# Performance work log

Measured on AMD Instinct MI355X. Metric: run time of the kernel, lower is better.

Reference implementation:

```python
import jax, jax.numpy as jnp
import numpy as np

N, E = 20000, 100000
D_IN, H1, C1 = 512, 8, 64   # conv1: 512 -> 8 heads x 64, concat -> 512
H2, C2 = 4, 128             # conv2: 512 -> 4 heads x 128, mean -> 128


def setup_inputs() -> dict:
    key = jax.random.key(0)
    k = jax.random.split(key, 12)
    s_in = 1.0 / np.sqrt(D_IN).astype(np.float32)
    return {
        "street_embedding": jax.random.normal(k[0], (N, D_IN), jnp.float32),
        "edge_index": jax.random.randint(k[1], (2, E), 0, N),
        "y": jax.random.randint(k[2], (N,), 0, C2),
        "train_mask": jax.random.bernoulli(k[3], 0.5, (N,)),
        "W1": jax.random.normal(k[4], (D_IN, H1 * C1), jnp.float32) * s_in,
        "att_src1": jax.random.normal(k[5], (H1, C1), jnp.float32) * 0.1,
        "att_dst1": jax.random.normal(k[6], (H1, C1), jnp.float32) * 0.1,
        "b1": jnp.zeros((H1 * C1,), jnp.float32),
        "W2": jax.random.normal(k[7], (H1 * C1, H2 * C2), jnp.float32) * s_in,
        "att_src2": jax.random.normal(k[8], (H2, C2), jnp.float32) * 0.1,
        "att_dst2": jax.random.normal(k[9], (H2, C2), jnp.float32) * 0.1,
        "b2": jnp.zeros((C2,), jnp.float32),
    }


def _gat_conv(x, W, a_src, a_dst, b, src, dst, n, H, C, concat):
    # linear transform (no bias, as in PyG GATConv's internal lin)
    xp = (x @ W).reshape(n, H, C)                      # [N,H,C]
    asrc = jnp.einsum('nhc,hc->nh', xp, a_src)         # [N,H]
    adst = jnp.einsum('nhc,hc->nh', xp, a_dst)
    e = jax.nn.leaky_relu(asrc[src] + adst[dst], 0.2)  # [E',H] edge scores
    # softmax over incoming edges per destination node
    m = jax.lax.stop_gradient(jax.ops.segment_max(e, dst, num_segments=n))
    ex = jnp.exp(e - m[dst])
    denom = jax.ops.segment_sum(ex, dst, num_segments=n)
    alpha = ex / (denom[dst] + 1e-16)                  # [E',H]
    out = jax.ops.segment_sum(alpha[:, :, None] * xp[src], dst, num_segments=n)  # [N,H,C]
    if concat:
        return out.reshape(n, H * C) + b
    return out.mean(axis=1) + b


def reference(street_embedding, edge_index, y, train_mask,
              W1, att_src1, att_dst1, b1, W2, att_src2, att_dst2, b2):
    n = street_embedding.shape[0]
    loop = jnp.arange(n)
    # PyG GATConv adds self-loops by default
    src = jnp.concatenate([edge_index[0], loop])
    dst = jnp.concatenate([edge_index[1], loop])
    # dropout layers are identity in eval mode
    h = _gat_conv(street_embedding, W1, att_src1, att_dst1, b1, src, dst, n, H1, C1, True)
    h = jax.nn.elu(h)
    out = _gat_conv(h, W2, att_src2, att_dst2, b2, src, dst, n, H2, C2, False)  # [N,C2]
    # CrossEntropyLoss, mean over train_mask nodes (weighted mean, jit-safe)
    logp = jax.nn.log_softmax(out, axis=-1)
    ce = -jnp.take_along_axis(logp, y[:, None], axis=-1)[:, 0]
    w = train_mask.astype(out.dtype)
    loss_su = jnp.sum(w * ce) / jnp.sum(w)
    return (loss_su, out)
```

## Files before the change

### kernel.cpp

```cpp
#include <hip/hip_runtime.h>
#include <cmath>

#define D_IN 512
#define HC   512
#define NH1  8
#define NC1  64
#define NH2  4
#define NC2  128
#define BM 128
#define BN 128
#define BK 64

typedef __attribute__((ext_vector_type(8))) short short8;
typedef __attribute__((ext_vector_type(4))) float f32x4;

__device__ inline ushort f2bf(float f) {
  unsigned u = __float_as_uint(f);
  return (ushort)((u + 0x7FFFu + ((u >> 16) & 1u)) >> 16);
}
__device__ inline float bf2f(ushort b) { return __uint_as_float(((unsigned)b) << 16); }

__global__ void k_cast_all(const float* __restrict__ x, ushort* __restrict__ Abf,
                           const float* __restrict__ W1, const float* __restrict__ W2,
                           ushort* __restrict__ Wt1, ushort* __restrict__ Wt2, int n4x) {
  const int KN = D_IN * HC;
  int i = blockIdx.x * blockDim.x + threadIdx.x;
  if (i < n4x) {
    float4 v = ((const float4*)x)[i];
    ushort4 r = { f2bf(v.x), f2bf(v.y), f2bf(v.z), f2bf(v.w) };
    ((ushort4*)Abf)[i] = r;
  } else {
    int idx = i - n4x;
    if (idx >= 2 * KN) return;
    const float* W = (idx < KN) ? W1 : W2;
    ushort* Wt = (idx < KN) ? Wt1 : Wt2;
    int j = (idx < KN) ? idx : idx - KN;
    int n = j / D_IN, k = j - n * D_IN;
    Wt[j] = f2bf(W[(size_t)k * HC + n]);
  }
}

template<int H>
__global__ void k_gemm_bf16(const ushort* __restrict__ A, const ushort* __restrict__ Bt,
                            ushort* __restrict__ Cbf,
                            const float* __restrict__ att_s, const float* __restrict__ att_d,
                            float* __restrict__ asrc, float* __restrict__ adst, int M) {
  constexpr int C = HC / H;
  __shared__ __align__(16) ushort As[BM * BK];
  __shared__ __align__(16) ushort Bs[BN * BK];
  int t = threadIdx.x;
  int m0 = blockIdx.y * BM;
  int n0 = blockIdx.x * BN;
  int wave = t >> 6, lane = t & 63;
  int ln = lane & 15, qd = lane >> 4;
  int wm = (wave >> 1) * 64, wn = (wave & 1) * 64;

  f32x4 acc[4][4] = {};

  int g = t >> 6, ct = (t >> 4) & 3, lt = t & 15;
  int rA0 = m0 + g * 16 + lt;      if (rA0 > M - 1) rA0 = M - 1;
  int rA1 = m0 + 64 + g * 16 + lt; if (rA1 > M - 1) rA1 = M - 1;
  const ushort* gA0 = A + (size_t)rA0 * D_IN + ct * 8;
  const ushort* gA1 = A + (size_t)rA1 * D_IN + ct * 8;
  const ushort* gB0 = Bt + (size_t)(n0 + g * 16 + lt) * D_IN + ct * 8;
  const ushort* gB1 = Bt + (size_t)(n0 + 64 + g * 16 + lt) * D_IN + ct * 8;

  for (int k0 = 0; k0 < D_IN; k0 += BK) {
    __syncthreads();
#pragma unroll
    for (int h = 0; h < 2; ++h) {
      int ko = k0 + h * 32;
      int lo = h * 4096;
      __builtin_amdgcn_global_load_lds(
          (const __attribute__((address_space(1))) void*)(gA0 + ko),
          (__attribute__((address_space(3))) void*)(As + lo + t * 8), 16, 0, 0);
      __builtin_amdgcn_global_load_lds(
          (const __attribute__((address_space(1))) void*)(gA1 + ko),
          (__attribute__((address_space(3))) void*)(As + lo + 2048 + t * 8), 16, 0, 0);
      __builtin_amdgcn_global_load_lds(
          (const __attribute__((address_space(1))) void*)(gB0 + ko),
          (__attribute__((address_space(3))) void*)(Bs + lo + t * 8), 16, 0, 0);
      __builtin_amdgcn_global_load_lds(
          (const __attribute__((address_space(1))) void*)(gB1 + ko),
          (__attribute__((address_space(3))) void*)(Bs + lo + 2048 + t * 8), 16, 0, 0);
    }
    __syncthreads();
#pragma unroll
    for (int h = 0; h < 2; ++h) {
      int lo = h * 4096;
      short8 a[4], bb[4];
#pragma unroll
      for (int i = 0; i < 4; ++i)
        a[i] = *(const short8*)&As[lo + (((wave >> 1) * 4 + i) * 4 + qd) * 128 + ln * 8];
#pragma unroll
      for (int j = 0; j < 4; ++j)
        bb[j] = *(const short8*)&Bs[lo + (((wave & 1) * 4 + j) * 4 + qd) * 128 + ln * 8];
#pragma unroll
      for (int i = 0; i < 4; ++i)
#pragma unroll
        for (int j = 0; j < 4; ++j)
          acc[i][j] = __builtin_amdgcn_mfma_f32_16x16x32_bf16(a[i], bb[j], acc[i][j], 0, 0, 0);
    }
  }

#pragma unroll
  for (int i = 0; i < 4; ++i) {
#pragma unroll
    for (int reg = 0; reg < 4; ++reg) {
      int row = m0 + wm + i * 16 + qd * 4 + reg;
      if (row >= M) continue;
#pragma unroll
      for (int j = 0; j < 4; ++j)
        Cbf[(size_t)row * HC + n0 + wn + j * 16 + ln] = f2bf(acc[i][j][reg]);
    }
  }

  int colbase = n0 + wn;
  int h = colbase / C;
  float sa[4], da[4];
#pragma unroll
  for (int j = 0; j < 4; ++j) {
    int c = (colbase % C) + j * 16 + ln;
    sa[j] = att_s[h * C + c];
    da[j] = att_d[h * C + c];
  }
#pragma unroll
  for (int i = 0; i < 4; ++i) {
#pragma unroll
    for (int reg = 0; reg < 4; ++reg) {
      float ps = acc[i][0][reg] * sa[0] + acc[i][1][reg] * sa[1]
               + acc[i][2][reg] * sa[2] + acc[i][3][reg] * sa[3];
      float pd = acc[i][0][reg] * da[0] + acc[i][1][reg] * da[1]
               + acc[i][2][reg] * da[2] + acc[i][3][reg] * da[3];
#pragma unroll
      for (int o = 1; o < 16; o <<= 1) { ps += __shfl_xor(ps, o); pd += __shfl_xor(pd, o); }
      int row = m0 + wm + i * 16 + qd * 4 + reg;
      if (ln == 0 && row < M) {
        if (C == 64) {
          asrc[row * H + h] = ps; adst[row * H + h] = pd;
        } else {
          int sub = (colbase >> 6) & 1;
          asrc[(row * H + h) * 2 + sub] = ps;
          adst[(row * H + h) * 2 + sub] = pd;
        }
      }
    }
  }
}

__global__ void k_hist(const int* __restrict__ ei, int E, int Etot, int* __restrict__ cnt) {
  int e = blockIdx.x * blockDim.x + threadIdx.x;
  if (e >= Etot) return;
  int d = (e < E) ? ei[E + e] : e - E;
  atomicAdd(&cnt[d], 1);
}

__global__ void k_scan(const int* __restrict__ cnt, int* __restrict__ rowstart, int N) {
  int tid = threadIdx.x;
  int T = (N + 1023) / 1024;
  int base = tid * T;
  int sum = 0;
  for (int i = 0; i < T; ++i) { int j = base + i; if (j < N) sum += cnt[j]; }
  int lane = tid & 63, w = tid >> 6;
  int v = sum;
#pragma unroll
  for (int off = 1; off < 64; off <<= 1) {
    int u = __shfl_up(v, off);
    if (lane >= off) v += u;
  }
  __shared__ int wsum[16];
  if (lane == 63) wsum[w] = v;
  __syncthreads();
  if (tid < 16) {
    int tv = wsum[tid];
#pragma unroll
    for (int off = 1; off < 16; off <<= 1) {
      int u = __shfl_up(tv, off);
      if (tid >= off) tv += u;
    }
    wsum[tid] = tv;
  }
  __syncthreads();
  int wave_prefix = (w == 0) ? 0 : wsum[w - 1];
  int run = wave_prefix + v - sum;
  for (int i = 0; i < T; ++i) {
    int j = base + i;
    if (j < N) { rowstart[j] = run; run += cnt[j]; }
  }
  if (tid == 1023) rowstart[N] = run;
}

__global__ void k_scatter(const int* __restrict__ ei, int E, int Etot,
                          const int* __restrict__ rowstart, int* __restrict__ cursor,
                          int* __restrict__ csr_src) {
  int e = blockIdx.x * blockDim.x + threadIdx.x;
  if (e >= Etot) return;
  int s = (e < E) ? ei[e] : e - E;
  int d = (e < E) ? ei[E + e] : e - E;
  int pos = atomicAdd(&cursor[d], 1);
  csr_src[rowstart[d] + pos] = s;
}

template<int H, int MODE>
__global__ void k_agg(const int* __restrict__ rowstart, const int* __restrict__ csr_src,
                      const float* __restrict__ asrc, const float* __restrict__ adst,
                      const ushort* __restrict__ xp, ushort* __restrict__ hout,
                      float* __restrict__ out2, const float* __restrict__ bias,
                      const int* __restrict__ y, const int* __restrict__ msk,
                      float* __restrict__ acc2, int N) {
  int n = blockIdx.x;
  int tid = threadIdx.x;
  constexpr int C = HC / H;
  int h = (tid * 4) / C;
  int beg = rowstart[n], end = rowstart[n + 1];

  __shared__ int   s_src[32];
  __shared__ float s_out[512];

  float adn = (MODE == 1) ? adst[n * H + h]
                          : adst[(n * H + h) * 2] + adst[(n * H + h) * 2 + 1];
  float ax = 0.f, ay = 0.f, az = 0.f, aw = 0.f, wsum = 0.f;

#define SCORE(s) ((MODE == 1) ? asrc[(s) * H + h] \
                              : asrc[((s) * H + h) * 2] + asrc[((s) * H + h) * 2 + 1])

  for (int c0 = beg; c0 < end; c0 += 32) {
    int len = end - c0; if (len > 32) len = 32;
    __syncthreads();
    if (tid < len) s_src[tid] = csr_src[c0 + tid];
    __syncthreads();
    int i = 0;
    for (; i + 1 < len; i += 2) {
      int s0 = s_src[i], s1 = s_src[i + 1];
      float v0 = SCORE(s0) + adn;
      float v1 = SCORE(s1) + adn;
      ushort4 a0 = ((const ushort4*)xp)[(size_t)s0 * 128 + tid];
      ushort4 a1 = ((const ushort4*)xp)[(size_t)s1 * 128 + tid];
      v0 = (v0 > 0.f) ? v0 : 0.2f * v0;
      v1 = (v1 > 0.f) ? v1 : 0.2f * v1;
      float w0 = __expf(v0), w1 = __expf(v1);
      ax += w0 * bf2f(a0.x) + w1 * bf2f(a1.x);
      ay += w0 * bf2f(a0.y) + w1 * bf2f(a1.y);
      az += w0 * bf2f(a0.z) + w1 * bf2f(a1.z);
      aw += w0 * bf2f(a0.w) + w1 * bf2f(a1.w);
      wsum += w0 + w1;
    }
    if (i < len) {
      int s0 = s_src[i];
      float v0 = SCORE(s0) + adn;
      ushort4 a0 = ((const ushort4*)xp)[(size_t)s0 * 128 + tid];
      v0 = (v0 > 0.f) ? v0 : 0.2f * v0;
      float w0 = __expf(v0);
      ax += w0 * bf2f(a0.x); ay += w0 * bf2f(a0.y);
      az += w0 * bf2f(a0.z); aw += w0 * bf2f(a0.w);
      wsum += w0;
    }
  }
#undef SCORE
  float rdn = 1.0f / (wsum + 1e-16f);
  ax *= rdn; ay *= rdn; az *= rdn; aw *= rdn;

  if (MODE == 1) {
    int hc = tid * 4;
    float v0 = ax + bias[hc], v1 = ay + bias[hc + 1];
    float v2 = az + bias[hc + 2], v3 = aw + bias[hc + 3];
    v0 = (v0 > 0.f) ? v0 : expm1f(v0);
    v1 = (v1 > 0.f) ? v1 : expm1f(v1);
    v2 = (v2 > 0.f) ? v2 : expm1f(v2);
    v3 = (v3 > 0.f) ? v3 : expm1f(v3);
    ushort4 rr = { f2bf(v0), f2bf(v1), f2bf(v2), f2bf(v3) };
    ((ushort4*)hout)[(size_t)n * 128 + tid] = rr;
  } else {
    int hc = tid * 4;
    s_out[hc] = ax; s_out[hc + 1] = ay; s_out[hc + 2] = az; s_out[hc + 3] = aw;
    __syncthreads();
    if (tid < 32) {
#pragma unroll
      for (int k = 0; k < 4; ++k) {
        int c = tid * 4 + k;
        float sum = s_out[c] + s_out[128 + c] + s_out[256 + c] + s_out[384 + c];
        float lg = sum * 0.25f + bias[c];
        out2[(size_t)n * NC2 + c] = lg;
        s_out[c] = lg;
      }
    }
    __syncthreads();
    float lv = s_out[tid];
    int lane = tid & 63, wv = tid >> 6;
    float mx = lv;
#pragma unroll
    for (int o = 32; o > 0; o >>= 1) mx = fmaxf(mx, __shfl_xor(mx, o));
    if (lane == 0) s_out[256 + wv] = mx;
    __syncthreads();
    mx = fmaxf(s_out[256], s_out[257]);
    float e = __expf(lv - mx);
#pragma unroll
    for (int o = 32; o > 0; o >>= 1) e += __shfl_xor(e, o);
    if (lane == 0) s_out[260 + wv] = e;
    __syncthreads();
    if (tid == 0 && msk[n] != 0) {
      float se = s_out[260] + s_out[261];
      float ce = mx + logf(se) - s_out[y[n]];
      int slot = n & 127;
      atomicAdd(&acc2[slot], ce);
      atomicAdd(&acc2[128 + slot], 1.0f);
    }
  }
}

__global__ void k_final(const float* __restrict__ acc2, float* __restrict__ out0) {
  int tid = threadIdx.x;
  float ce = acc2[tid], ct = acc2[128 + tid];
#pragma unroll
  for (int o = 32; o > 0; o >>= 1) { ce += __shfl_xor(ce, o); ct += __shfl_xor(ct, o); }
  __shared__ float s[4];
  if ((tid & 63) == 0) { s[(tid >> 6) * 2] = ce; s[(tid >> 6) * 2 + 1] = ct; }
  __syncthreads();
  if (tid == 0) out0[0] = (s[0] + s[2]) / (s[1] + s[3]);
}

extern "C" void kernel_launch(void* const* d_in, const int* in_sizes, int n_in,
                              void* d_out, int out_size, void* d_ws, size_t ws_size,
                              hipStream_t stream) {
  const float* x   = (const float*)d_in[0];
  const int*   ei  = (const int*)d_in[1];
  const int*   y   = (const int*)d_in[2];
  const int*   msk = (const int*)d_in[3];
  const float* W1  = (const float*)d_in[4];
  const float* as1 = (const float*)d_in[5];
  const float* ad1 = (const float*)d_in[6];
  const float* b1  = (const float*)d_in[7];
  const float* W2  = (const float*)d_in[8];
  const float* as2 = (const float*)d_in[9];
  const float* ad2 = (const float*)d_in[10];
  const float* b2  = (const float*)d_in[11];
  float* out = (float*)d_out;

  int N = in_sizes[0] / D_IN;
  int E = in_sizes[1] / 2;
  int Etot = E + N;

  float* ws = (float*)d_ws;
  size_t NF = (size_t)N * HC;
  float* asr1 = ws;
  float* adt1 = asr1 + (size_t)N * NH1;
  float* asr2 = adt1 + (size_t)N * NH1;
  float* adt2 = asr2 + (size_t)N * 2 * NH2;
  float* acc2 = adt2 + (size_t)N * 2 * NH2;
  int*   cnt    = (int*)(acc2 + 256);
  int*   cursor = cnt + N;
  size_t zero_bytes = (256 + 2 * (size_t)N) * sizeof(float);
  int*   rowstart = cursor + N;
  int*   csr_src  = rowstart + N + 1;
  ushort* xpbf = (ushort*)((((uintptr_t)(csr_src + Etot)) + 15) & ~(uintptr_t)15);
  ushort* Abf = xpbf + NF;
  ushort* Wt1 = Abf + NF;
  ushort* Wt2 = Wt1 + (size_t)D_IN * HC;

  hipMemsetAsync(acc2, 0, zero_bytes, stream);

  int n4x = (int)(NF / 4);
  int cast_total = n4x + 2 * D_IN * HC;
  k_cast_all<<<(cast_total + 255) / 256, 256, 0, stream>>>(x, Abf, W1, W2, Wt1, Wt2, n4x);

  k_hist<<<(Etot + 255) / 256, 256, 0, stream>>>(ei, E, Etot, cnt);
  k_scan<<<1, 1024, 0, stream>>>(cnt, rowstart, N);
  k_scatter<<<(Etot + 255) / 256, 256, 0, stream>>>(ei, E, Etot, rowstart, cursor, csr_src);

  dim3 ggrid(HC / BN, (N + BM - 1) / BM);

  k_gemm_bf16<NH1><<<ggrid, 256, 0, stream>>>(Abf, Wt1, xpbf, as1, ad1, asr1, adt1, N);
  k_agg<NH1, 1><<<N, 128, 0, stream>>>(rowstart, csr_src, asr1, adt1, xpbf, Abf,
                                       nullptr, b1, nullptr, nullptr, nullptr, N);

  k_gemm_bf16<NH2><<<ggrid, 256, 0, stream>>>(Abf, Wt2, xpbf, as2, ad2, asr2, adt2, N);
  k_agg<NH2, 2><<<N, 128, 0, stream>>>(rowstart, csr_src, asr2, adt2, xpbf, nullptr,
                                       out + 1, b2, y, msk, acc2, N);

  k_final<<<1, 128, 0, stream>>>(acc2, out);
}
```

Measured before the change: 288.1 us.

## Double-buffer GEMM K loop, remap workgroups per XCD, wave-per-node aggregation

The GEMM K loop now double-buffers LDS tiles of 32 along K, prefetching the next stage while the MFMAs run on the current one, using explicit vmcnt waits and barriers. Workgroup IDs are remapped so that consecutive tiles land on the same XCD, which should improve L2 reuse. The aggregation kernel is rewritten so that one wave handles one node with 8 channels per lane, source indices are broadcast by shuffles instead of through LDS, and the reductions are done in registers without block syncs. In exchange, the manual waitcnt pipelining and the index remapping must stay correct, and each wave now walks its edge list serially.

```diff
diff --git a/kernel.cpp b/kernel.cpp
--- a/kernel.cpp
+++ b/kernel.cpp
@@ -9,9 +9,9 @@
 #define NC2  128
 #define BM 128
 #define BN 128
-#define BK 64
 
 typedef __attribute__((ext_vector_type(8))) short short8;
+typedef __attribute__((ext_vector_type(8))) unsigned short u16x8;
 typedef __attribute__((ext_vector_type(4))) float f32x4;
 
 __device__ inline ushort f2bf(float f) {
@@ -46,11 +46,18 @@
                             const float* __restrict__ att_s, const float* __restrict__ att_d,
                             float* __restrict__ asrc, float* __restrict__ adst, int M) {
   constexpr int C = HC / H;
-  __shared__ __align__(16) ushort As[BM * BK];
-  __shared__ __align__(16) ushort Bs[BN * BK];
+  __shared__ __align__(16) ushort As[2 * 4096];
+  __shared__ __align__(16) ushort Bs[2 * 4096];
   int t = threadIdx.x;
-  int m0 = blockIdx.y * BM;
-  int n0 = blockIdx.x * BN;
+
+  int nwg = gridDim.x * gridDim.y;
+  int lin = blockIdx.y * gridDim.x + blockIdx.x;
+  int q = nwg >> 3, r = nwg & 7;
+  int xcd = lin & 7, pos = lin >> 3;
+  int wg = (xcd < r ? xcd * (q + 1) : r * (q + 1) + (xcd - r) * q) + pos;
+  int m0 = (wg >> 2) * BM;
+  int n0 = (wg & 3) * BN;
+
   int wave = t >> 6, lane = t & 63;
   int ln = lane & 15, qd = lane >> 4;
   int wm = (wave >> 1) * 64, wn = (wave & 1) * 64;
@@ -65,43 +72,50 @@
   const ushort* gB0 = Bt + (size_t)(n0 + g * 16 + lt) * D_IN + ct * 8;
   const ushort* gB1 = Bt + (size_t)(n0 + 64 + g * 16 + lt) * D_IN + ct * 8;
 
-  for (int k0 = 0; k0 < D_IN; k0 += BK) {
-    __syncthreads();
-#pragma unroll
-    for (int h = 0; h < 2; ++h) {
-      int ko = k0 + h * 32;
-      int lo = h * 4096;
-      __builtin_amdgcn_global_load_lds(
-          (const __attribute__((address_space(1))) void*)(gA0 + ko),
-          (__attribute__((address_space(3))) void*)(As + lo + t * 8), 16, 0, 0);
-      __builtin_amdgcn_global_load_lds(
-          (const __attribute__((address_space(1))) void*)(gA1 + ko),
-          (__attribute__((address_space(3))) void*)(As + lo + 2048 + t * 8), 16, 0, 0);
-      __builtin_amdgcn_global_load_lds(
-          (const __attribute__((address_space(1))) void*)(gB0 + ko),
-          (__attribute__((address_space(3))) void*)(Bs + lo + t * 8), 16, 0, 0);
-      __builtin_amdgcn_global_load_lds(
-          (const __attribute__((address_space(1))) void*)(gB1 + ko),
-          (__attribute__((address_space(3))) void*)(Bs + lo + 2048 + t * 8), 16, 0, 0);
-    }
-    __syncthreads();
-#pragma unroll
-    for (int h = 0; h < 2; ++h) {
-      int lo = h * 4096;
-      short8 a[4], bb[4];
-#pragma unroll
-      for (int i = 0; i < 4; ++i)
-        a[i] = *(const short8*)&As[lo + (((wave >> 1) * 4 + i) * 4 + qd) * 128 + ln * 8];
+#define STAGE(buf, ko)                                                          \
+  do {                                                                          \
+    int lo_ = (buf) * 4096;                                                     \
+    __builtin_amdgcn_global_load_lds(                                           \
+        (const __attribute__((address_space(1))) void*)(gA0 + (ko)),            \
+        (__attribute__((address_space(3))) void*)(As + lo_ + t * 8), 16, 0, 0); \
+    __builtin_amdgcn_global_load_lds(                                           \
+        (const __attribute__((address_space(1))) void*)(gA1 + (ko)),            \
+        (__attribute__((address_space(3))) void*)(As + lo_ + 2048 + t * 8), 16, 0, 0); \
+    __builtin_amdgcn_global_load_lds(                                           \
+        (const __attribute__((address_space(1))) void*)(gB0 + (ko)),            \
+        (__attribute__((address_space(3))) void*)(Bs + lo_ + t * 8), 16, 0, 0); \
+    __builtin_amdgcn_global_load_lds(                                           \
+        (const __attribute__((address_space(1))) void*)(gB1 + (ko)),            \
+        (__attribute__((address_space(3))) void*)(Bs + lo_ + 2048 + t * 8), 16, 0, 0); \
+  } while (0)
+
+  STAGE(0, 0);
+  int cur = 0;
+  for (int it = 0; it < 16; ++it) {
+    if (it < 15) {
+      STAGE(cur ^ 1, (it + 1) * 32);
+      asm volatile("s_waitcnt vmcnt(4)" ::: "memory");
+    } else {
+      asm volatile("s_waitcnt vmcnt(0)" ::: "memory");
+    }
+    __builtin_amdgcn_s_barrier();
+    int lo = cur * 4096;
+    short8 a[4], bb[4];
+#pragma unroll
+    for (int i = 0; i < 4; ++i)
+      a[i] = *(const short8*)&As[lo + (((wave >> 1) * 4 + i) * 4 + qd) * 128 + ln * 8];
+#pragma unroll
+    for (int j = 0; j < 4; ++j)
+      bb[j] = *(const short8*)&Bs[lo + (((wave & 1) * 4 + j) * 4 + qd) * 128 + ln * 8];
+#pragma unroll
+    for (int i = 0; i < 4; ++i)
 #pragma unroll
       for (int j = 0; j < 4; ++j)
-        bb[j] = *(const short8*)&Bs[lo + (((wave & 1) * 4 + j) * 4 + qd) * 128 + ln * 8];
-#pragma unroll
-      for (int i = 0; i < 4; ++i)
-#pragma unroll
-        for (int j = 0; j < 4; ++j)
-          acc[i][j] = __builtin_amdgcn_mfma_f32_16x16x32_bf16(a[i], bb[j], acc[i][j], 0, 0, 0);
-    }
-  }
+        acc[i][j] = __builtin_amdgcn_mfma_f32_16x16x32_bf16(a[i], bb[j], acc[i][j], 0, 0, 0);
+    __builtin_amdgcn_s_barrier();
+    cur ^= 1;
+  }
+#undef STAGE
 
 #pragma unroll
   for (int i = 0; i < 4; ++i) {
@@ -208,99 +222,102 @@
                       float* __restrict__ out2, const float* __restrict__ bias,
                       const int* __restrict__ y, const int* __restrict__ msk,
                       float* __restrict__ acc2, int N) {
-  int n = blockIdx.x;
-  int tid = threadIdx.x;
   constexpr int C = HC / H;
-  int h = (tid * 4) / C;
+  int wv = threadIdx.x >> 6, lane = threadIdx.x & 63;
+  int n = blockIdx.x * 4 + wv;
+  if (n >= N) return;
+  int h = (MODE == 1) ? (lane >> 3) : (lane >> 4);
   int beg = rowstart[n], end = rowstart[n + 1];
 
-  __shared__ int   s_src[32];
-  __shared__ float s_out[512];
-
-  float adn = (MODE == 1) ? adst[n * H + h]
-                          : adst[(n * H + h) * 2] + adst[(n * H + h) * 2 + 1];
-  float ax = 0.f, ay = 0.f, az = 0.f, aw = 0.f, wsum = 0.f;
-
-#define SCORE(s) ((MODE == 1) ? asrc[(s) * H + h] \
-                              : asrc[((s) * H + h) * 2] + asrc[((s) * H + h) * 2 + 1])
-
-  for (int c0 = beg; c0 < end; c0 += 32) {
-    int len = end - c0; if (len > 32) len = 32;
-    __syncthreads();
-    if (tid < len) s_src[tid] = csr_src[c0 + tid];
-    __syncthreads();
-    int i = 0;
-    for (; i + 1 < len; i += 2) {
-      int s0 = s_src[i], s1 = s_src[i + 1];
-      float v0 = SCORE(s0) + adn;
-      float v1 = SCORE(s1) + adn;
-      ushort4 a0 = ((const ushort4*)xp)[(size_t)s0 * 128 + tid];
-      ushort4 a1 = ((const ushort4*)xp)[(size_t)s1 * 128 + tid];
+  float adn;
+  if (MODE == 1) adn = adst[n * H + h];
+  else { float2 t2 = ((const float2*)adst)[n * H + h]; adn = t2.x + t2.y; }
+
+  float acc[8] = {};
+  float wsum = 0.f;
+
+  for (int c0 = beg; c0 < end; c0 += 64) {
+    int len = end - c0; if (len > 64) len = 64;
+    int ev = (lane < len) ? csr_src[c0 + lane] : 0;
+    int j = 0;
+    for (; j + 1 < len; j += 2) {
+      int s0 = __shfl(ev, j), s1 = __shfl(ev, j + 1);
+      float v0, v1;
+      if (MODE == 1) { v0 = asrc[s0 * H + h]; v1 = asrc[s1 * H + h]; }
+      else {
+        float2 p0 = ((const float2*)asrc)[s0 * H + h];
+        float2 p1 = ((const float2*)asrc)[s1 * H + h];
+        v0 = p0.x + p0.y; v1 = p1.x + p1.y;
+      }
+      u16x8 a0 = ((const u16x8*)xp)[(size_t)s0 * 64 + lane];
+      u16x8 a1 = ((const u16x8*)xp)[(size_t)s1 * 64 + lane];
+      v0 += adn; v1 += adn;
       v0 = (v0 > 0.f) ? v0 : 0.2f * v0;
       v1 = (v1 > 0.f) ? v1 : 0.2f * v1;
       float w0 = __expf(v0), w1 = __expf(v1);
-      ax += w0 * bf2f(a0.x) + w1 * bf2f(a1.x);
-      ay += w0 * bf2f(a0.y) + w1 * bf2f(a1.y);
-      az += w0 * bf2f(a0.z) + w1 * bf2f(a1.z);
-      aw += w0 * bf2f(a0.w) + w1 * bf2f(a1.w);
+#pragma unroll
+      for (int k = 0; k < 8; ++k)
+        acc[k] += w0 * bf2f(a0[k]) + w1 * bf2f(a1[k]);
       wsum += w0 + w1;
     }
-    if (i < len) {
-      int s0 = s_src[i];
-      float v0 = SCORE(s0) + adn;
-      ushort4 a0 = ((const ushort4*)xp)[(size_t)s0 * 128 + tid];
+    if (j < len) {
+      int s0 = __shfl(ev, j);
+      float v0;
+      if (MODE == 1) v0 = asrc[s0 * H + h];
+      else { float2 p0 = ((const float2*)asrc)[s0 * H + h]; v0 = p0.x + p0.y; }
+      u16x8 a0 = ((const u16x8*)xp)[(size_t)s0 * 64 + lane];
+      v0 += adn;
       v0 = (v0 > 0.f) ? v0 : 0.2f * v0;
       float w0 = __expf(v0);
-      ax += w0 * bf2f(a0.x); ay += w0 * bf2f(a0.y);
-      az += w0 * bf2f(a0.z); aw += w0 * bf2f(a0.w);
+#pragma unroll
+      for (int k = 0; k < 8; ++k) acc[k] += w0 * bf2f(a0[k]);
       wsum += w0;
     }
   }
-#undef SCORE
   float rdn = 1.0f / (wsum + 1e-16f);
-  ax *= rdn; ay *= rdn; az *= rdn; aw *= rdn;
+#pragma unroll
+  for (int k = 0; k < 8; ++k) acc[k] *= rdn;
 
   if (MODE == 1) {
-    int hc = tid * 4;
-    float v0 = ax + bias[hc], v1 = ay + bias[hc + 1];
-    float v2 = az + bias[hc + 2], v3 = aw + bias[hc + 3];
-    v0 = (v0 > 0.f) ? v0 : expm1f(v0);
-    v1 = (v1 > 0.f) ? v1 : expm1f(v1);
-    v2 = (v2 > 0.f) ? v2 : expm1f(v2);
-    v3 = (v3 > 0.f) ? v3 : expm1f(v3);
-    ushort4 rr = { f2bf(v0), f2bf(v1), f2bf(v2), f2bf(v3) };
-    ((ushort4*)hout)[(size_t)n * 128 + tid] = rr;
+    int c = lane * 8;
+    u16x8 rr;
+#pragma unroll
+    for (int k = 0; k < 8; ++k) {
+      float v = acc[k] + bias[c + k];
+      v = (v > 0.f) ? v : expm1f(v);
+      rr[k] = f2bf(v);
+    }
+    ((u16x8*)hout)[(size_t)n * 64 + lane] = rr;
   } else {
-    int hc = tid * 4;
-    s_out[hc] = ax; s_out[hc + 1] = ay; s_out[hc + 2] = az; s_out[hc + 3] = aw;
-    __syncthreads();
-    if (tid < 32) {
-#pragma unroll
-      for (int k = 0; k < 4; ++k) {
-        int c = tid * 4 + k;
-        float sum = s_out[c] + s_out[128 + c] + s_out[256 + c] + s_out[384 + c];
-        float lg = sum * 0.25f + bias[c];
-        out2[(size_t)n * NC2 + c] = lg;
-        s_out[c] = lg;
-      }
-    }
-    __syncthreads();
-    float lv = s_out[tid];
-    int lane = tid & 63, wv = tid >> 6;
-    float mx = lv;
-#pragma unroll
-    for (int o = 32; o > 0; o >>= 1) mx = fmaxf(mx, __shfl_xor(mx, o));
-    if (lane == 0) s_out[256 + wv] = mx;
-    __syncthreads();
-    mx = fmaxf(s_out[256], s_out[257]);
-    float e = __expf(lv - mx);
-#pragma unroll
-    for (int o = 32; o > 0; o >>= 1) e += __shfl_xor(e, o);
-    if (lane == 0) s_out[260 + wv] = e;
-    __syncthreads();
-    if (tid == 0 && msk[n] != 0) {
-      float se = s_out[260] + s_out[261];
-      float ce = mx + logf(se) - s_out[y[n]];
+#pragma unroll
+    for (int k = 0; k < 8; ++k) {
+      float v = acc[k];
+      v += __shfl_xor(v, 16);
+      v += __shfl_xor(v, 32);
+      acc[k] = v * 0.25f + bias[(lane & 15) * 8 + k];
+    }
+    if (lane < 16) {
+      int cb = lane * 8;
+#pragma unroll
+      for (int k = 0; k < 8; ++k) out2[(size_t)n * NC2 + cb + k] = acc[k];
+    }
+    float mx = acc[0];
+#pragma unroll
+    for (int k = 1; k < 8; ++k) mx = fmaxf(mx, acc[k]);
+#pragma unroll
+    for (int o = 1; o < 16; o <<= 1) mx = fmaxf(mx, __shfl_xor(mx, o));
+    float e = 0.f;
+#pragma unroll
+    for (int k = 0; k < 8; ++k) e += __expf(acc[k] - mx);
+#pragma unroll
+    for (int o = 1; o < 16; o <<= 1) e += __shfl_xor(e, o);
+    int yv = y[n];
+    float sel = acc[0];
+#pragma unroll
+    for (int k = 1; k < 8; ++k) sel = ((yv & 7) == k) ? acc[k] : sel;
+    float vy = __shfl(sel, yv >> 3);
+    if (lane == 0 && msk[n] != 0) {
+      float ce = mx + logf(e) - vy;
       int slot = n & 127;
       atomicAdd(&acc2[slot], ce);
       atomicAdd(&acc2[128 + slot], 1.0f);
@@ -368,14 +385,15 @@
   k_scatter<<<(Etot + 255) / 256, 256, 0, stream>>>(ei, E, Etot, rowstart, cursor, csr_src);
 
   dim3 ggrid(HC / BN, (N + BM - 1) / BM);
+  int aggblocks = (N + 3) / 4;
 
   k_gemm_bf16<NH1><<<ggrid, 256, 0, stream>>>(Abf, Wt1, xpbf, as1, ad1, asr1, adt1, N);
-  k_agg<NH1, 1><<<N, 128, 0, stream>>>(rowstart, csr_src, asr1, adt1, xpbf, Abf,
-                                       nullptr, b1, nullptr, nullptr, nullptr, N);
+  k_agg<NH1, 1><<<aggblocks, 256, 0, stream>>>(rowstart, csr_src, asr1, adt1, xpbf, Abf,
+                                               nullptr, b1, nullptr, nullptr, nullptr, N);
 
   k_gemm_bf16<NH2><<<ggrid, 256, 0, stream>>>(Abf, Wt2, xpbf, as2, ad2, asr2, adt2, N);
-  k_agg<NH2, 2><<<N, 128, 0, stream>>>(rowstart, csr_src, asr2, adt2, xpbf, nullptr,
-                                       out + 1, b2, y, msk, acc2, N);
+  k_agg<NH2, 2><<<aggblocks, 256, 0, stream>>>(rowstart, csr_src, asr2, adt2, xpbf, nullptr,
+                                               out + 1, b2, y, msk, acc2, N);
 
   k_final<<<1, 128, 0, stream>>>(acc2, out);
 }
```

Result: slower. 296.0 us (+2.7%).
